# Optimization experiments

Hardware: AMD Instinct MI355X
Metric: run time of the kernel (lower is better)

The kernel has to match this reference:

```python
import jax, jax.numpy as jnp
import numpy as np

EPS = 1e-5

def _bn(x, g, b, m, v):
    # inference batchnorm: (x - mean) * rsqrt(var + eps) * gamma + beta
    return (x - m) * jax.lax.rsqrt(v + EPS) * g + b

def _relu6(x):
    return jnp.clip(x, 0.0, 6.0)

def setup_inputs() -> dict:
    key = jax.random.key(0)
    ks = jax.random.split(key, 20)
    N, Cin, Cout, K = 200000, 32, 32, 9  # K = 3^2 kernel offsets (dimension=2)
    H = int(round(Cin * 6))              # hidden = in_channels * expand_ratio = 192
    inp = {}
    inp["feats"] = jax.random.normal(ks[0], (N, Cin), jnp.float32)
    # rulebook neighbor map: -1 means no active neighbor at that kernel offset
    inp["neighbor_idx"] = jax.random.randint(ks[1], (N, K), -1, N, dtype=jnp.int32)
    # ME convs have bias=False by default
    inp["W1"] = jax.random.normal(ks[2], (Cin, H), jnp.float32) * 0.05
    inp["W2"] = jax.random.normal(ks[3], (K, H), jnp.float32) * 0.05   # channelwise (depthwise) kernel
    inp["W3"] = jax.random.normal(ks[4], (H, Cout), jnp.float32) * 0.05
    for i, (name, c) in enumerate([("1", H), ("2", H), ("3", Cout)]):
        base = 5 + 4 * i
        inp["g" + name] = 1.0 + 0.1 * jax.random.normal(ks[base], (c,), jnp.float32)
        inp["b" + name] = 0.1 * jax.random.normal(ks[base + 1], (c,), jnp.float32)
        inp["m" + name] = 0.1 * jax.random.normal(ks[base + 2], (c,), jnp.float32)
        inp["v" + name] = jax.random.uniform(ks[base + 3], (c,), jnp.float32, 0.5, 1.5)
    return inp

def _depthwise_sparse_conv(x, neighbor_idx, W2):
    # x: [N, H], neighbor_idx: [N, K] (-1 = missing), W2: [K, H]
    K = W2.shape[0]
    acc = jnp.zeros_like(x)
    safe = jnp.maximum(neighbor_idx, 0)
    valid = (neighbor_idx >= 0)
    for k in range(K):  # small fixed kernel loop; each gather streams [N, H]
        g = jnp.where(valid[:, k:k + 1], x[safe[:, k]], 0.0)
        acc = acc + g * W2[k]
    return acc

def reference(feats, neighbor_idx, W1, W2, W3,
              g1, b1, m1, v1, g2, b2, m2, v2, g3, b3, m3, v3):
    identity = feats
    x = _relu6(_bn(feats @ W1, g1, b1, m1, v1))          # 1x1 expand conv
    x = _depthwise_sparse_conv(x, neighbor_idx, W2)       # 3x3 depthwise sparse conv
    x = _relu6(_bn(x, g2, b2, m2, v2))
    x = _bn(x @ W3, g3, b3, m3, v3)                       # 1x1 project conv
    return x + identity                                   # residual (in==out, stride==1)
```

## Files before the change

### kernel.cpp

```cpp
#include <hip/hip_runtime.h>

#define EPS 1e-5f

typedef __bf16 bf16x8 __attribute__((ext_vector_type(8)));
typedef float f32x4 __attribute__((ext_vector_type(4)));

union BF8 { bf16x8 v; unsigned short u[8]; uint4 q; };

__device__ inline unsigned short f32_to_bf16(float f) {
    unsigned u = __builtin_bit_cast(unsigned, f);
    return (unsigned short)((u + 0x7FFFu + ((u >> 16) & 1u)) >> 16);
}
__device__ inline float relu6f(float x) { return fminf(fmaxf(x, 0.f), 6.f); }

__global__ __launch_bounds__(256) void k0_prep(
    const float* __restrict__ W1, const float* __restrict__ W3,
    const float* __restrict__ g1, const float* __restrict__ b1,
    const float* __restrict__ m1, const float* __restrict__ v1,
    const float* __restrict__ g2, const float* __restrict__ b2,
    const float* __restrict__ m2, const float* __restrict__ v2,
    const float* __restrict__ g3, const float* __restrict__ b3,
    const float* __restrict__ m3, const float* __restrict__ v3,
    unsigned short* __restrict__ w1t, unsigned short* __restrict__ w3t,
    float* __restrict__ bnc)
{
    const int gtid = blockIdx.x * 256 + threadIdx.x;
    const int gstr = gridDim.x * 256;
    for (int i = gtid; i < 6144; i += gstr) {
        int n = i >> 5, k = i & 31;
        w1t[i] = f32_to_bf16(W1[k * 192 + n]);
    }
    for (int i = gtid; i < 6144; i += gstr) {
        int n = i / 192, k = i - n * 192;
        w3t[i] = f32_to_bf16(W3[k * 32 + n]);
    }
    if (blockIdx.x == 0) {
        int t = threadIdx.x;
        const float Q = 255.f / 6.f;
        if (t < 192) {
            float s = g1[t] * rsqrtf(v1[t] + EPS);
            bnc[t] = s * Q; bnc[192 + t] = (b1[t] - m1[t] * s) * Q;
            float u = g2[t] * rsqrtf(v2[t] + EPS);
            bnc[384 + t] = u; bnc[576 + t] = b2[t] - m2[t] * u;
            if (t < 32) {
                float w = g3[t] * rsqrtf(v3[t] + EPS);
                bnc[768 + t] = w; bnc[800 + t] = b3[t] - m3[t] * w;
            }
        }
    }
}

__global__ __launch_bounds__(256) void k1_expand(
    const float* __restrict__ feats, const unsigned short* __restrict__ w1t,
    const float* __restrict__ bnc, unsigned char* __restrict__ x1, int N)
{
    __shared__ __align__(16) unsigned outB[128 * 52];
    const int tid = threadIdx.x;
    const int rowbase = blockIdx.x * 128;
    const int lane = tid & 63, wave = tid >> 6;
    const int m = lane & 15, q = lane >> 4;

    bf16x8 bf[12];
#pragma unroll
    for (int t = 0; t < 12; ++t)
        bf[t] = *(const bf16x8*)(w1t + (16 * t + m) * 32 + q * 8);

#pragma unroll
    for (int p = 0; p < 2; ++p) {
        const int tile = wave * 2 + p;
        const int row = rowbase + tile * 16 + m;
        float4 f0 = {0.f,0.f,0.f,0.f}, f1 = {0.f,0.f,0.f,0.f};
        if (row < N) {
            f0 = *(const float4*)(feats + (size_t)row * 32 + q * 8);
            f1 = *(const float4*)(feats + (size_t)row * 32 + q * 8 + 4);
        }
        BF8 af;
        af.u[0] = f32_to_bf16(f0.x); af.u[1] = f32_to_bf16(f0.y);
        af.u[2] = f32_to_bf16(f0.z); af.u[3] = f32_to_bf16(f0.w);
        af.u[4] = f32_to_bf16(f1.x); af.u[5] = f32_to_bf16(f1.y);
        af.u[6] = f32_to_bf16(f1.z); af.u[7] = f32_to_bf16(f1.w);

        f32x4 acc[12];
#pragma unroll
        for (int t = 0; t < 12; ++t) {
            f32x4 z = {0.f, 0.f, 0.f, 0.f};
            acc[t] = __builtin_amdgcn_mfma_f32_16x16x32_bf16(bf[t], af.v, z, 0, 0, 0);
        }

        const int rl = tile * 16 + m;
#pragma unroll
        for (int t = 0; t < 12; ++t) {
            float4 sv = *(const float4*)(bnc + 16 * t + 4 * q);
            float4 bv = *(const float4*)(bnc + 192 + 16 * t + 4 * q);
            float y0 = fminf(fmaxf(fmaf(acc[t][0], sv.x, bv.x), 0.f), 255.f);
            float y1 = fminf(fmaxf(fmaf(acc[t][1], sv.y, bv.y), 0.f), 255.f);
            float y2 = fminf(fmaxf(fmaf(acc[t][2], sv.z, bv.z), 0.f), 255.f);
            float y3 = fminf(fmaxf(fmaf(acc[t][3], sv.w, bv.w), 0.f), 255.f);
            unsigned d = (unsigned)(y0 + 0.5f)
                       | ((unsigned)(y1 + 0.5f) << 8)
                       | ((unsigned)(y2 + 0.5f) << 16)
                       | ((unsigned)(y3 + 0.5f) << 24);
            outB[rl * 52 + 4 * t + q] = d;
        }
    }
    __syncthreads();

#pragma unroll
    for (int j = 0; j < 6; ++j) {
        int i = j * 256 + tid;
        int r = i / 12, c = i % 12;
        int gr = rowbase + r;
        if (gr < N)
            *(uint4*)(x1 + (size_t)gr * 192 + c * 16) = *(const uint4*)(&outB[r * 52 + c * 4]);
    }
}

__global__ __launch_bounds__(192) void k2_fused(
    const unsigned char* __restrict__ x1, const int* __restrict__ nbr,
    const float* __restrict__ W2, const unsigned short* __restrict__ w3t,
    const float* __restrict__ bnc, const float* __restrict__ feats,
    float* __restrict__ out, int N)
{
    __shared__ __align__(16) unsigned short x2L[48 * 200];
    __shared__ __align__(16) int offL[48 * 12];
    const int tid = threadIdx.x;
    const int rowbase = blockIdx.x * 48;

    for (int i = tid; i < 432; i += 192) {
        int r = i / 9, k = i - r * 9;
        int n = rowbase + r;
        int idx = (n < N) ? nbr[(size_t)n * 9 + k] : -1;
        offL[r * 12 + k] = (idx < 0) ? -1 : idx * 192;
    }

    const int cg = tid % 48;
    const int slot = tid / 48;
    const int c0 = cg * 4;
    const char* x1b = (const char*)x1 + c0;

    const float DQ = 6.f / 255.f;
    float w2v[9][4];
#pragma unroll
    for (int k = 0; k < 9; ++k) {
        float4 w = *(const float4*)(W2 + k * 192 + c0);
        w2v[k][0] = w.x * DQ; w2v[k][1] = w.y * DQ; w2v[k][2] = w.z * DQ; w2v[k][3] = w.w * DQ;
    }
    float4 s2 = *(const float4*)(bnc + 384 + c0);
    float4 bb2 = *(const float4*)(bnc + 576 + c0);
    __syncthreads();

#pragma unroll
    for (int it = 0; it < 6; ++it) {
        int r0 = it * 8 + slot, r1 = r0 + 4;
        const int* nA = &offL[r0 * 12];
        const int* nB = &offL[r1 * 12];
        int4 a03 = *(const int4*)nA; int4 a47 = *(const int4*)(nA + 4); int a8 = nA[8];
        int4 b03 = *(const int4*)nB; int4 b47 = *(const int4*)(nB + 4); int b8 = nB[8];
        int offA[9] = {a03.x, a03.y, a03.z, a03.w, a47.x, a47.y, a47.z, a47.w, a8};
        int offB[9] = {b03.x, b03.y, b03.z, b03.w, b47.x, b47.y, b47.z, b47.w, b8};
        unsigned gA[9], gB[9];
#pragma unroll
        for (int k = 0; k < 9; ++k) {
            gA[k] = *(const unsigned*)(x1b + (offA[k] < 0 ? 0 : offA[k]));
            gB[k] = *(const unsigned*)(x1b + (offB[k] < 0 ? 0 : offB[k]));
        }
        float a0 = 0.f, a1 = 0.f, a2 = 0.f, a3 = 0.f;
        float c0f = 0.f, c1 = 0.f, c2 = 0.f, c3 = 0.f;
#pragma unroll
        for (int k = 0; k < 9; ++k) {
            unsigned ga = offA[k] >= 0 ? gA[k] : 0u;
            unsigned gb = offB[k] >= 0 ? gB[k] : 0u;
            a0 = fmaf((float)(ga & 0xFF),         w2v[k][0], a0);
            a1 = fmaf((float)((ga >> 8) & 0xFF),  w2v[k][1], a1);
            a2 = fmaf((float)((ga >> 16) & 0xFF), w2v[k][2], a2);
            a3 = fmaf((float)(ga >> 24),          w2v[k][3], a3);
            c0f = fmaf((float)(gb & 0xFF),         w2v[k][0], c0f);
            c1  = fmaf((float)((gb >> 8) & 0xFF),  w2v[k][1], c1);
            c2  = fmaf((float)((gb >> 16) & 0xFF), w2v[k][2], c2);
            c3  = fmaf((float)(gb >> 24),          w2v[k][3], c3);
        }
        a0 = relu6f(fmaf(a0, s2.x, bb2.x));
        a1 = relu6f(fmaf(a1, s2.y, bb2.y));
        a2 = relu6f(fmaf(a2, s2.z, bb2.z));
        a3 = relu6f(fmaf(a3, s2.w, bb2.w));
        c0f = relu6f(fmaf(c0f, s2.x, bb2.x));
        c1  = relu6f(fmaf(c1,  s2.y, bb2.y));
        c2  = relu6f(fmaf(c2,  s2.z, bb2.z));
        c3  = relu6f(fmaf(c3,  s2.w, bb2.w));
        uint2 pA, pB;
        pA.x = (unsigned)f32_to_bf16(a0) | ((unsigned)f32_to_bf16(a1) << 16);
        pA.y = (unsigned)f32_to_bf16(a2) | ((unsigned)f32_to_bf16(a3) << 16);
        pB.x = (unsigned)f32_to_bf16(c0f) | ((unsigned)f32_to_bf16(c1) << 16);
        pB.y = (unsigned)f32_to_bf16(c2)  | ((unsigned)f32_to_bf16(c3) << 16);
        *(uint2*)(&x2L[r0 * 200 + c0]) = pA;
        *(uint2*)(&x2L[r1 * 200 + c0]) = pB;
    }
    __syncthreads();

    const int lane = tid & 63;
    const int wave = tid >> 6;
    const int m = lane & 15;
    const int q = lane >> 4;

    bf16x8 bfrag[12];
#pragma unroll
    for (int s = 0; s < 6; ++s)
#pragma unroll
        for (int t = 0; t < 2; ++t)
            bfrag[s * 2 + t] = *(const bf16x8*)(w3t + (16 * t + m) * 192 + 32 * s + q * 8);

    f32x4 acc0 = {0.f, 0.f, 0.f, 0.f}, acc1 = {0.f, 0.f, 0.f, 0.f};
    const int rw = wave * 16;
#pragma unroll
    for (int s = 0; s < 6; ++s) {
        bf16x8 a = *reinterpret_cast<const bf16x8*>(&x2L[(rw + m) * 200 + 32 * s + q * 8]);
        acc0 = __builtin_amdgcn_mfma_f32_16x16x32_bf16(a, bfrag[s * 2 + 0], acc0, 0, 0, 0);
        acc1 = __builtin_amdgcn_mfma_f32_16x16x32_bf16(a, bfrag[s * 2 + 1], acc1, 0, 0, 0);
    }

#pragma unroll
    for (int t = 0; t < 2; ++t) {
        f32x4 acc = (t == 0) ? acc0 : acc1;
        int c = 16 * t + m;
        float s3 = bnc[768 + c], bb3 = bnc[800 + c];
#pragma unroll
        for (int i = 0; i < 4; ++i) {
            int r = rowbase + rw + q * 4 + i;
            if (r < N) {
                int o = r * 32 + c;
                out[o] = fmaf(acc[i], s3, bb3) + feats[o];
            }
        }
    }
}

extern "C" void kernel_launch(void* const* d_in, const int* in_sizes, int n_in,
                              void* d_out, int out_size, void* d_ws, size_t ws_size,
                              hipStream_t stream) {
    const float* feats = (const float*)d_in[0];
    const int*   nbr   = (const int*)d_in[1];
    const float* W1    = (const float*)d_in[2];
    const float* W2    = (const float*)d_in[3];
    const float* W3    = (const float*)d_in[4];
    const float* g1 = (const float*)d_in[5];
    const float* b1 = (const float*)d_in[6];
    const float* m1 = (const float*)d_in[7];
    const float* v1 = (const float*)d_in[8];
    const float* g2 = (const float*)d_in[9];
    const float* b2 = (const float*)d_in[10];
    const float* m2 = (const float*)d_in[11];
    const float* v2 = (const float*)d_in[12];
    const float* g3 = (const float*)d_in[13];
    const float* b3 = (const float*)d_in[14];
    const float* m3 = (const float*)d_in[15];
    const float* v3 = (const float*)d_in[16];
    float* out = (float*)d_out;

    const int N = in_sizes[0] / 32;

    char* ws = (char*)d_ws;
    unsigned char*  x1  = (unsigned char*)ws;
    unsigned short* w1t = (unsigned short*)(ws + (size_t)N * 192);
    unsigned short* w3t = w1t + 6144;
    float*          bnc = (float*)(w3t + 6144);

    k0_prep<<<dim3(32), dim3(256), 0, stream>>>(
        W1, W3, g1, b1, m1, v1, g2, b2, m2, v2, g3, b3, m3, v3, w1t, w3t, bnc);
    k1_expand<<<dim3((N + 127) / 128), dim3(256), 0, stream>>>(
        feats, w1t, bnc, x1, N);
    k2_fused<<<dim3((N + 47) / 48), dim3(192), 0, stream>>>(
        x1, nbr, W2, w3t, bnc, feats, out, N);
}
```

Measured before the change: 200.5 us.

## Fuse prep, expand and depthwise/project kernels into one cooperative persistent kernel

Replaces the three kernel launches with a single cooperative persistent kernel. Each block first computes the BN constants and bf16 weight fragments itself, runs a grid-stride expand phase into the uint8 workspace, does a grid-wide sync, then runs the gather, depthwise and project phase grid-stride. The aim is to remove launch gaps and the separate prep kernel. In exchange it adds a grid barrier, tiles phase one at 96 rows with 192 threads, and recomputes the weight conversion in every block.

```diff
diff --git a/kernel.cpp b/kernel.cpp
--- a/kernel.cpp
+++ b/kernel.cpp
@@ -1,4 +1,7 @@
 #include <hip/hip_runtime.h>
+#include <hip/hip_cooperative_groups.h>
+
+namespace coopg = cooperative_groups;
 
 #define EPS 1e-5f
 
@@ -13,129 +16,101 @@
 }
 __device__ inline float relu6f(float x) { return fminf(fmaxf(x, 0.f), 6.f); }
 
-__global__ __launch_bounds__(256) void k0_prep(
-    const float* __restrict__ W1, const float* __restrict__ W3,
+__global__ __launch_bounds__(192) void fused(
+    const float* __restrict__ feats, const int* __restrict__ nbr,
+    const float* __restrict__ W1, const float* __restrict__ W2,
+    const float* __restrict__ W3,
     const float* __restrict__ g1, const float* __restrict__ b1,
     const float* __restrict__ m1, const float* __restrict__ v1,
     const float* __restrict__ g2, const float* __restrict__ b2,
     const float* __restrict__ m2, const float* __restrict__ v2,
     const float* __restrict__ g3, const float* __restrict__ b3,
     const float* __restrict__ m3, const float* __restrict__ v3,
-    unsigned short* __restrict__ w1t, unsigned short* __restrict__ w3t,
-    float* __restrict__ bnc)
+    unsigned char* __restrict__ x1, float* __restrict__ out,
+    int N, int nt1, int nt2)
 {
-    const int gtid = blockIdx.x * 256 + threadIdx.x;
-    const int gstr = gridDim.x * 256;
-    for (int i = gtid; i < 6144; i += gstr) {
-        int n = i >> 5, k = i & 31;
-        w1t[i] = f32_to_bf16(W1[k * 192 + n]);
-    }
-    for (int i = gtid; i < 6144; i += gstr) {
-        int n = i / 192, k = i - n * 192;
-        w3t[i] = f32_to_bf16(W3[k * 32 + n]);
-    }
-    if (blockIdx.x == 0) {
-        int t = threadIdx.x;
-        const float Q = 255.f / 6.f;
-        if (t < 192) {
-            float s = g1[t] * rsqrtf(v1[t] + EPS);
-            bnc[t] = s * Q; bnc[192 + t] = (b1[t] - m1[t] * s) * Q;
-            float u = g2[t] * rsqrtf(v2[t] + EPS);
-            bnc[384 + t] = u; bnc[576 + t] = b2[t] - m2[t] * u;
-            if (t < 32) {
-                float w = g3[t] * rsqrtf(v3[t] + EPS);
-                bnc[768 + t] = w; bnc[800 + t] = b3[t] - m3[t] * w;
-            }
-        }
-    }
-}
-
-__global__ __launch_bounds__(256) void k1_expand(
-    const float* __restrict__ feats, const unsigned short* __restrict__ w1t,
-    const float* __restrict__ bnc, unsigned char* __restrict__ x1, int N)
-{
-    __shared__ __align__(16) unsigned outB[128 * 52];
-    const int tid = threadIdx.x;
-    const int rowbase = blockIdx.x * 128;
+    __shared__ __align__(16) char sh[21504];
+    unsigned*       outB = (unsigned*)sh;
+    float*          bn1  = (float*)(sh + 19968);
+    unsigned short* x2L  = (unsigned short*)sh;
+    int*            offL = (int*)(sh + 19200);
+
+    const int tid  = threadIdx.x;
     const int lane = tid & 63, wave = tid >> 6;
     const int m = lane & 15, q = lane >> 4;
 
-    bf16x8 bf[12];
+    {
+        const float Q = 255.f / 6.f;
+        int c = tid;
+        float s = g1[c] * rsqrtf(v1[c] + EPS);
+        bn1[c]       = s * Q;
+        bn1[192 + c] = (b1[c] - m1[c] * s) * Q;
+    }
+    BF8 bf[12];
 #pragma unroll
     for (int t = 0; t < 12; ++t)
-        bf[t] = *(const bf16x8*)(w1t + (16 * t + m) * 32 + q * 8);
-
-#pragma unroll
-    for (int p = 0; p < 2; ++p) {
-        const int tile = wave * 2 + p;
-        const int row = rowbase + tile * 16 + m;
-        float4 f0 = {0.f,0.f,0.f,0.f}, f1 = {0.f,0.f,0.f,0.f};
-        if (row < N) {
-            f0 = *(const float4*)(feats + (size_t)row * 32 + q * 8);
-            f1 = *(const float4*)(feats + (size_t)row * 32 + q * 8 + 4);
-        }
-        BF8 af;
-        af.u[0] = f32_to_bf16(f0.x); af.u[1] = f32_to_bf16(f0.y);
-        af.u[2] = f32_to_bf16(f0.z); af.u[3] = f32_to_bf16(f0.w);
-        af.u[4] = f32_to_bf16(f1.x); af.u[5] = f32_to_bf16(f1.y);
-        af.u[6] = f32_to_bf16(f1.z); af.u[7] = f32_to_bf16(f1.w);
-
-        f32x4 acc[12];
-#pragma unroll
-        for (int t = 0; t < 12; ++t) {
-            f32x4 z = {0.f, 0.f, 0.f, 0.f};
-            acc[t] = __builtin_amdgcn_mfma_f32_16x16x32_bf16(bf[t], af.v, z, 0, 0, 0);
-        }
-
-        const int rl = tile * 16 + m;
-#pragma unroll
-        for (int t = 0; t < 12; ++t) {
-            float4 sv = *(const float4*)(bnc + 16 * t + 4 * q);
-            float4 bv = *(const float4*)(bnc + 192 + 16 * t + 4 * q);
-            float y0 = fminf(fmaxf(fmaf(acc[t][0], sv.x, bv.x), 0.f), 255.f);
-            float y1 = fminf(fmaxf(fmaf(acc[t][1], sv.y, bv.y), 0.f), 255.f);
-            float y2 = fminf(fmaxf(fmaf(acc[t][2], sv.z, bv.z), 0.f), 255.f);
-            float y3 = fminf(fmaxf(fmaf(acc[t][3], sv.w, bv.w), 0.f), 255.f);
-            unsigned d = (unsigned)(y0 + 0.5f)
-                       | ((unsigned)(y1 + 0.5f) << 8)
-                       | ((unsigned)(y2 + 0.5f) << 16)
-                       | ((unsigned)(y3 + 0.5f) << 24);
-            outB[rl * 52 + 4 * t + q] = d;
-        }
-    }
+#pragma unroll
+        for (int j = 0; j < 8; ++j)
+            bf[t].u[j] = f32_to_bf16(W1[(q * 8 + j) * 192 + 16 * t + m]);
     __syncthreads();
 
-#pragma unroll
-    for (int j = 0; j < 6; ++j) {
-        int i = j * 256 + tid;
-        int r = i / 12, c = i % 12;
-        int gr = rowbase + r;
-        if (gr < N)
-            *(uint4*)(x1 + (size_t)gr * 192 + c * 16) = *(const uint4*)(&outB[r * 52 + c * 4]);
-    }
-}
-
-__global__ __launch_bounds__(192) void k2_fused(
-    const unsigned char* __restrict__ x1, const int* __restrict__ nbr,
-    const float* __restrict__ W2, const unsigned short* __restrict__ w3t,
-    const float* __restrict__ bnc, const float* __restrict__ feats,
-    float* __restrict__ out, int N)
-{
-    __shared__ __align__(16) unsigned short x2L[48 * 200];
-    __shared__ __align__(16) int offL[48 * 12];
-    const int tid = threadIdx.x;
-    const int rowbase = blockIdx.x * 48;
-
-    for (int i = tid; i < 432; i += 192) {
-        int r = i / 9, k = i - r * 9;
-        int n = rowbase + r;
-        int idx = (n < N) ? nbr[(size_t)n * 9 + k] : -1;
-        offL[r * 12 + k] = (idx < 0) ? -1 : idx * 192;
-    }
-
-    const int cg = tid % 48;
+    for (int tb = blockIdx.x; tb < nt1; tb += gridDim.x) {
+        const int rowbase = tb * 96;
+#pragma unroll
+        for (int p = 0; p < 2; ++p) {
+            const int tile = wave * 2 + p;
+            const int row = rowbase + tile * 16 + m;
+            float4 f0 = {0.f,0.f,0.f,0.f}, f1 = {0.f,0.f,0.f,0.f};
+            if (row < N) {
+                f0 = *(const float4*)(feats + (size_t)row * 32 + q * 8);
+                f1 = *(const float4*)(feats + (size_t)row * 32 + q * 8 + 4);
+            }
+            BF8 af;
+            af.u[0] = f32_to_bf16(f0.x); af.u[1] = f32_to_bf16(f0.y);
+            af.u[2] = f32_to_bf16(f0.z); af.u[3] = f32_to_bf16(f0.w);
+            af.u[4] = f32_to_bf16(f1.x); af.u[5] = f32_to_bf16(f1.y);
+            af.u[6] = f32_to_bf16(f1.z); af.u[7] = f32_to_bf16(f1.w);
+
+            f32x4 acc[12];
+#pragma unroll
+            for (int t = 0; t < 12; ++t) {
+                f32x4 z = {0.f, 0.f, 0.f, 0.f};
+                acc[t] = __builtin_amdgcn_mfma_f32_16x16x32_bf16(bf[t].v, af.v, z, 0, 0, 0);
+            }
+
+            const int rl = tile * 16 + m;
+#pragma unroll
+            for (int t = 0; t < 12; ++t) {
+                float4 sv = *(const float4*)(bn1 + 16 * t + 4 * q);
+                float4 bv = *(const float4*)(bn1 + 192 + 16 * t + 4 * q);
+                float y0 = fminf(fmaxf(fmaf(acc[t][0], sv.x, bv.x), 0.f), 255.f);
+                float y1 = fminf(fmaxf(fmaf(acc[t][1], sv.y, bv.y), 0.f), 255.f);
+                float y2 = fminf(fmaxf(fmaf(acc[t][2], sv.z, bv.z), 0.f), 255.f);
+                float y3 = fminf(fmaxf(fmaf(acc[t][3], sv.w, bv.w), 0.f), 255.f);
+                unsigned d = (unsigned)(y0 + 0.5f)
+                           | ((unsigned)(y1 + 0.5f) << 8)
+                           | ((unsigned)(y2 + 0.5f) << 16)
+                           | ((unsigned)(y3 + 0.5f) << 24);
+                outB[rl * 52 + 4 * t + q] = d;
+            }
+        }
+        __syncthreads();
+#pragma unroll
+        for (int j = 0; j < 6; ++j) {
+            int i = j * 192 + tid;
+            int r = i / 12, c = i % 12;
+            int gr = rowbase + r;
+            if (gr < N)
+                *(uint4*)(x1 + (size_t)gr * 192 + c * 16) = *(const uint4*)(&outB[r * 52 + c * 4]);
+        }
+        __syncthreads();
+    }
+
+    coopg::this_grid().sync();
+
+    const int cg48 = tid % 48;
     const int slot = tid / 48;
-    const int c0 = cg * 4;
+    const int c0 = cg48 * 4;
     const char* x1b = (const char*)x1 + c0;
 
     const float DQ = 6.f / 255.f;
@@ -145,90 +120,109 @@
         float4 w = *(const float4*)(W2 + k * 192 + c0);
         w2v[k][0] = w.x * DQ; w2v[k][1] = w.y * DQ; w2v[k][2] = w.z * DQ; w2v[k][3] = w.w * DQ;
     }
-    float4 s2 = *(const float4*)(bnc + 384 + c0);
-    float4 bb2 = *(const float4*)(bnc + 576 + c0);
-    __syncthreads();
-
-#pragma unroll
-    for (int it = 0; it < 6; ++it) {
-        int r0 = it * 8 + slot, r1 = r0 + 4;
-        const int* nA = &offL[r0 * 12];
-        const int* nB = &offL[r1 * 12];
-        int4 a03 = *(const int4*)nA; int4 a47 = *(const int4*)(nA + 4); int a8 = nA[8];
-        int4 b03 = *(const int4*)nB; int4 b47 = *(const int4*)(nB + 4); int b8 = nB[8];
-        int offA[9] = {a03.x, a03.y, a03.z, a03.w, a47.x, a47.y, a47.z, a47.w, a8};
-        int offB[9] = {b03.x, b03.y, b03.z, b03.w, b47.x, b47.y, b47.z, b47.w, b8};
-        unsigned gA[9], gB[9];
-#pragma unroll
-        for (int k = 0; k < 9; ++k) {
-            gA[k] = *(const unsigned*)(x1b + (offA[k] < 0 ? 0 : offA[k]));
-            gB[k] = *(const unsigned*)(x1b + (offB[k] < 0 ? 0 : offB[k]));
-        }
-        float a0 = 0.f, a1 = 0.f, a2 = 0.f, a3 = 0.f;
-        float c0f = 0.f, c1 = 0.f, c2 = 0.f, c3 = 0.f;
-#pragma unroll
-        for (int k = 0; k < 9; ++k) {
-            unsigned ga = offA[k] >= 0 ? gA[k] : 0u;
-            unsigned gb = offB[k] >= 0 ? gB[k] : 0u;
-            a0 = fmaf((float)(ga & 0xFF),         w2v[k][0], a0);
-            a1 = fmaf((float)((ga >> 8) & 0xFF),  w2v[k][1], a1);
-            a2 = fmaf((float)((ga >> 16) & 0xFF), w2v[k][2], a2);
-            a3 = fmaf((float)(ga >> 24),          w2v[k][3], a3);
-            c0f = fmaf((float)(gb & 0xFF),         w2v[k][0], c0f);
-            c1  = fmaf((float)((gb >> 8) & 0xFF),  w2v[k][1], c1);
-            c2  = fmaf((float)((gb >> 16) & 0xFF), w2v[k][2], c2);
-            c3  = fmaf((float)(gb >> 24),          w2v[k][3], c3);
-        }
-        a0 = relu6f(fmaf(a0, s2.x, bb2.x));
-        a1 = relu6f(fmaf(a1, s2.y, bb2.y));
-        a2 = relu6f(fmaf(a2, s2.z, bb2.z));
-        a3 = relu6f(fmaf(a3, s2.w, bb2.w));
-        c0f = relu6f(fmaf(c0f, s2.x, bb2.x));
-        c1  = relu6f(fmaf(c1,  s2.y, bb2.y));
-        c2  = relu6f(fmaf(c2,  s2.z, bb2.z));
-        c3  = relu6f(fmaf(c3,  s2.w, bb2.w));
-        uint2 pA, pB;
-        pA.x = (unsigned)f32_to_bf16(a0) | ((unsigned)f32_to_bf16(a1) << 16);
-        pA.y = (unsigned)f32_to_bf16(a2) | ((unsigned)f32_to_bf16(a3) << 16);
-        pB.x = (unsigned)f32_to_bf16(c0f) | ((unsigned)f32_to_bf16(c1) << 16);
-        pB.y = (unsigned)f32_to_bf16(c2)  | ((unsigned)f32_to_bf16(c3) << 16);
-        *(uint2*)(&x2L[r0 * 200 + c0]) = pA;
-        *(uint2*)(&x2L[r1 * 200 + c0]) = pB;
-    }
-    __syncthreads();
-
-    const int lane = tid & 63;
-    const int wave = tid >> 6;
-    const int m = lane & 15;
-    const int q = lane >> 4;
-
-    bf16x8 bfrag[12];
+    float4 s2, bb2;
+    {
+        float4 gv = *(const float4*)(g2 + c0), bv = *(const float4*)(b2 + c0);
+        float4 mv = *(const float4*)(m2 + c0), vv = *(const float4*)(v2 + c0);
+        s2.x = gv.x * rsqrtf(vv.x + EPS); bb2.x = bv.x - mv.x * s2.x;
+        s2.y = gv.y * rsqrtf(vv.y + EPS); bb2.y = bv.y - mv.y * s2.y;
+        s2.z = gv.z * rsqrtf(vv.z + EPS); bb2.z = bv.z - mv.z * s2.z;
+        s2.w = gv.w * rsqrtf(vv.w + EPS); bb2.w = bv.w - mv.w * s2.w;
+    }
+    BF8 bfrag[12];
 #pragma unroll
     for (int s = 0; s < 6; ++s)
 #pragma unroll
         for (int t = 0; t < 2; ++t)
-            bfrag[s * 2 + t] = *(const bf16x8*)(w3t + (16 * t + m) * 192 + 32 * s + q * 8);
-
-    f32x4 acc0 = {0.f, 0.f, 0.f, 0.f}, acc1 = {0.f, 0.f, 0.f, 0.f};
-    const int rw = wave * 16;
-#pragma unroll
-    for (int s = 0; s < 6; ++s) {
-        bf16x8 a = *reinterpret_cast<const bf16x8*>(&x2L[(rw + m) * 200 + 32 * s + q * 8]);
-        acc0 = __builtin_amdgcn_mfma_f32_16x16x32_bf16(a, bfrag[s * 2 + 0], acc0, 0, 0, 0);
-        acc1 = __builtin_amdgcn_mfma_f32_16x16x32_bf16(a, bfrag[s * 2 + 1], acc1, 0, 0, 0);
-    }
-
+#pragma unroll
+            for (int j = 0; j < 8; ++j)
+                bfrag[s * 2 + t].u[j] = f32_to_bf16(W3[(32 * s + q * 8 + j) * 32 + 16 * t + m]);
+    float s3v[2], bb3v[2];
 #pragma unroll
     for (int t = 0; t < 2; ++t) {
-        f32x4 acc = (t == 0) ? acc0 : acc1;
         int c = 16 * t + m;
-        float s3 = bnc[768 + c], bb3 = bnc[800 + c];
-#pragma unroll
-        for (int i = 0; i < 4; ++i) {
-            int r = rowbase + rw + q * 4 + i;
-            if (r < N) {
-                int o = r * 32 + c;
-                out[o] = fmaf(acc[i], s3, bb3) + feats[o];
+        float w = g3[c] * rsqrtf(v3[c] + EPS);
+        s3v[t] = w; bb3v[t] = b3[c] - m3[c] * w;
+    }
+
+    for (int tb = blockIdx.x; tb < nt2; tb += gridDim.x) {
+        const int rowbase = tb * 48;
+        for (int i = tid; i < 432; i += 192) {
+            int r = i / 9, k = i - r * 9;
+            int n = rowbase + r;
+            int idx = (n < N) ? nbr[(size_t)n * 9 + k] : -1;
+            offL[r * 12 + k] = (idx < 0) ? -1 : idx * 192;
+        }
+        __syncthreads();
+
+#pragma unroll
+        for (int it = 0; it < 6; ++it) {
+            int r0 = it * 8 + slot, r1 = r0 + 4;
+            const int* nA = &offL[r0 * 12];
+            const int* nB = &offL[r1 * 12];
+            int4 a03 = *(const int4*)nA; int4 a47 = *(const int4*)(nA + 4); int a8 = nA[8];
+            int4 b03 = *(const int4*)nB; int4 b47 = *(const int4*)(nB + 4); int b8 = nB[8];
+            int offA[9] = {a03.x, a03.y, a03.z, a03.w, a47.x, a47.y, a47.z, a47.w, a8};
+            int offB[9] = {b03.x, b03.y, b03.z, b03.w, b47.x, b47.y, b47.z, b47.w, b8};
+            unsigned gA[9], gB[9];
+#pragma unroll
+            for (int k = 0; k < 9; ++k) {
+                gA[k] = *(const unsigned*)(x1b + (offA[k] < 0 ? 0 : offA[k]));
+                gB[k] = *(const unsigned*)(x1b + (offB[k] < 0 ? 0 : offB[k]));
+            }
+            float a0 = 0.f, a1 = 0.f, a2 = 0.f, a3 = 0.f;
+            float c0f = 0.f, c1 = 0.f, c2 = 0.f, c3 = 0.f;
+#pragma unroll
+            for (int k = 0; k < 9; ++k) {
+                unsigned ga = offA[k] >= 0 ? gA[k] : 0u;
+                unsigned gb = offB[k] >= 0 ? gB[k] : 0u;
+                a0 = fmaf((float)(ga & 0xFF),         w2v[k][0], a0);
+                a1 = fmaf((float)((ga >> 8) & 0xFF),  w2v[k][1], a1);
+                a2 = fmaf((float)((ga >> 16) & 0xFF), w2v[k][2], a2);
+                a3 = fmaf((float)(ga >> 24),          w2v[k][3], a3);
+                c0f = fmaf((float)(gb & 0xFF),         w2v[k][0], c0f);
+                c1  = fmaf((float)((gb >> 8) & 0xFF),  w2v[k][1], c1);
+                c2  = fmaf((float)((gb >> 16) & 0xFF), w2v[k][2], c2);
+                c3  = fmaf((float)(gb >> 24),          w2v[k][3], c3);
+            }
+            a0 = relu6f(fmaf(a0, s2.x, bb2.x));
+            a1 = relu6f(fmaf(a1, s2.y, bb2.y));
+            a2 = relu6f(fmaf(a2, s2.z, bb2.z));
+            a3 = relu6f(fmaf(a3, s2.w, bb2.w));
+            c0f = relu6f(fmaf(c0f, s2.x, bb2.x));
+            c1  = relu6f(fmaf(c1,  s2.y, bb2.y));
+            c2  = relu6f(fmaf(c2,  s2.z, bb2.z));
+            c3  = relu6f(fmaf(c3,  s2.w, bb2.w));
+            uint2 pA, pB;
+            pA.x = (unsigned)f32_to_bf16(a0) | ((unsigned)f32_to_bf16(a1) << 16);
+            pA.y = (unsigned)f32_to_bf16(a2) | ((unsigned)f32_to_bf16(a3) << 16);
+            pB.x = (unsigned)f32_to_bf16(c0f) | ((unsigned)f32_to_bf16(c1) << 16);
+            pB.y = (unsigned)f32_to_bf16(c2)  | ((unsigned)f32_to_bf16(c3) << 16);
+            *(uint2*)(&x2L[r0 * 200 + c0]) = pA;
+            *(uint2*)(&x2L[r1 * 200 + c0]) = pB;
+        }
+        __syncthreads();
+
+        f32x4 acc0 = {0.f, 0.f, 0.f, 0.f}, acc1 = {0.f, 0.f, 0.f, 0.f};
+        const int rw = wave * 16;
+#pragma unroll
+        for (int s = 0; s < 6; ++s) {
+            bf16x8 a = *reinterpret_cast<const bf16x8*>(&x2L[(rw + m) * 200 + 32 * s + q * 8]);
+            acc0 = __builtin_amdgcn_mfma_f32_16x16x32_bf16(a, bfrag[s * 2 + 0].v, acc0, 0, 0, 0);
+            acc1 = __builtin_amdgcn_mfma_f32_16x16x32_bf16(a, bfrag[s * 2 + 1].v, acc1, 0, 0, 0);
+        }
+
+#pragma unroll
+        for (int t = 0; t < 2; ++t) {
+            f32x4 acc = (t == 0) ? acc0 : acc1;
+            int c = 16 * t + m;
+#pragma unroll
+            for (int i = 0; i < 4; ++i) {
+                int r = rowbase + rw + q * 4 + i;
+                if (r < N) {
+                    int o = r * 32 + c;
+                    out[o] = fmaf(acc[i], s3v[t], bb3v[t]) + feats[o];
+                }
             }
         }
     }
@@ -257,17 +251,30 @@
     float* out = (float*)d_out;
 
     const int N = in_sizes[0] / 32;
-
-    char* ws = (char*)d_ws;
-    unsigned char*  x1  = (unsigned char*)ws;
-    unsigned short* w1t = (unsigned short*)(ws + (size_t)N * 192);
-    unsigned short* w3t = w1t + 6144;
-    float*          bnc = (float*)(w3t + 6144);
-
-    k0_prep<<<dim3(32), dim3(256), 0, stream>>>(
-        W1, W3, g1, b1, m1, v1, g2, b2, m2, v2, g3, b3, m3, v3, w1t, w3t, bnc);
-    k1_expand<<<dim3((N + 127) / 128), dim3(256), 0, stream>>>(
-        feats, w1t, bnc, x1, N);
-    k2_fused<<<dim3((N + 47) / 48), dim3(192), 0, stream>>>(
-        x1, nbr, W2, w3t, bnc, feats, out, N);
+    int nt1 = (N + 95) / 96;
+    int nt2 = (N + 47) / 48;
+
+    unsigned char* x1 = (unsigned char*)d_ws;
+
+    static int s_grid = -1;
+    if (s_grid < 0) {
+        int dev = 0; hipGetDevice(&dev);
+        int cus = 256;
+        hipDeviceGetAttribute(&cus, hipDeviceAttributeMultiprocessorCount, dev);
+        int occ = 0;
+        hipOccupancyMaxActiveBlocksPerMultiprocessor(&occ, fused, 192, 0);
+        if (occ < 1) occ = 1;
+        s_grid = occ * cus;
+    }
+    int maxt = (nt1 > nt2) ? nt1 : nt2;
+    int grid = (s_grid < maxt) ? s_grid : maxt;
+
+    void* args[] = {
+        (void*)&feats, (void*)&nbr, (void*)&W1, (void*)&W2, (void*)&W3,
+        (void*)&g1, (void*)&b1, (void*)&m1, (void*)&v1,
+        (void*)&g2, (void*)&b2, (void*)&m2, (void*)&v2,
+        (void*)&g3, (void*)&b3, (void*)&m3, (void*)&v3,
+        (void*)&x1, (void*)&out, (void*)&N, (void*)&nt1, (void*)&nt2
+    };
+    hipLaunchCooperativeKernel(fused, dim3(grid), dim3(192), args, 0u, stream);
 }
```

After: 327.1 us. 63.2% more time.

## Drop prep kernel and compute weight conversion and BN constants in consumer kernels

Applied to the files above, without the earlier changes.

Removes the separate k0_prep launch and instead converts W1/W3 to bf16 and folds the batchnorm constants inside each block of the expand and fused kernels. The expand kernel also drops its LDS staging buffer and writes packed uint8 activations straight to global memory with 4-byte stores. This saves one kernel launch and its serialization, but adds redundant strided weight loads and conversions in every block and replaces coalesced 16-byte stores with narrower scattered ones.

```diff
diff --git a/kernel.cpp b/kernel.cpp
--- a/kernel.cpp
+++ b/kernel.cpp
@@ -13,57 +13,32 @@
 }
 __device__ inline float relu6f(float x) { return fminf(fmaxf(x, 0.f), 6.f); }
 
-__global__ __launch_bounds__(256) void k0_prep(
-    const float* __restrict__ W1, const float* __restrict__ W3,
+__global__ __launch_bounds__(256) void k1_expand(
+    const float* __restrict__ feats, const float* __restrict__ W1,
     const float* __restrict__ g1, const float* __restrict__ b1,
     const float* __restrict__ m1, const float* __restrict__ v1,
-    const float* __restrict__ g2, const float* __restrict__ b2,
-    const float* __restrict__ m2, const float* __restrict__ v2,
-    const float* __restrict__ g3, const float* __restrict__ b3,
-    const float* __restrict__ m3, const float* __restrict__ v3,
-    unsigned short* __restrict__ w1t, unsigned short* __restrict__ w3t,
-    float* __restrict__ bnc)
+    unsigned char* __restrict__ x1, int N)
 {
-    const int gtid = blockIdx.x * 256 + threadIdx.x;
-    const int gstr = gridDim.x * 256;
-    for (int i = gtid; i < 6144; i += gstr) {
-        int n = i >> 5, k = i & 31;
-        w1t[i] = f32_to_bf16(W1[k * 192 + n]);
-    }
-    for (int i = gtid; i < 6144; i += gstr) {
-        int n = i / 192, k = i - n * 192;
-        w3t[i] = f32_to_bf16(W3[k * 32 + n]);
-    }
-    if (blockIdx.x == 0) {
-        int t = threadIdx.x;
-        const float Q = 255.f / 6.f;
-        if (t < 192) {
-            float s = g1[t] * rsqrtf(v1[t] + EPS);
-            bnc[t] = s * Q; bnc[192 + t] = (b1[t] - m1[t] * s) * Q;
-            float u = g2[t] * rsqrtf(v2[t] + EPS);
-            bnc[384 + t] = u; bnc[576 + t] = b2[t] - m2[t] * u;
-            if (t < 32) {
-                float w = g3[t] * rsqrtf(v3[t] + EPS);
-                bnc[768 + t] = w; bnc[800 + t] = b3[t] - m3[t] * w;
-            }
-        }
-    }
-}
-
-__global__ __launch_bounds__(256) void k1_expand(
-    const float* __restrict__ feats, const unsigned short* __restrict__ w1t,
-    const float* __restrict__ bnc, unsigned char* __restrict__ x1, int N)
-{
-    __shared__ __align__(16) unsigned outB[128 * 52];
+    __shared__ __align__(16) float bn1[384];
     const int tid = threadIdx.x;
     const int rowbase = blockIdx.x * 128;
     const int lane = tid & 63, wave = tid >> 6;
     const int m = lane & 15, q = lane >> 4;
 
-    bf16x8 bf[12];
+    if (tid < 192) {
+        const float Q = 255.f / 6.f;
+        float s = g1[tid] * rsqrtf(v1[tid] + EPS);
+        bn1[tid]       = s * Q;
+        bn1[192 + tid] = (b1[tid] - m1[tid] * s) * Q;
+    }
+
+    BF8 bf[12];
 #pragma unroll
     for (int t = 0; t < 12; ++t)
-        bf[t] = *(const bf16x8*)(w1t + (16 * t + m) * 32 + q * 8);
+#pragma unroll
+        for (int j = 0; j < 8; ++j)
+            bf[t].u[j] = f32_to_bf16(W1[(q * 8 + j) * 192 + 16 * t + m]);
+    __syncthreads();
 
 #pragma unroll
     for (int p = 0; p < 2; ++p) {
@@ -84,42 +59,37 @@
 #pragma unroll
         for (int t = 0; t < 12; ++t) {
             f32x4 z = {0.f, 0.f, 0.f, 0.f};
-            acc[t] = __builtin_amdgcn_mfma_f32_16x16x32_bf16(bf[t], af.v, z, 0, 0, 0);
-        }
-
-        const int rl = tile * 16 + m;
-#pragma unroll
-        for (int t = 0; t < 12; ++t) {
-            float4 sv = *(const float4*)(bnc + 16 * t + 4 * q);
-            float4 bv = *(const float4*)(bnc + 192 + 16 * t + 4 * q);
-            float y0 = fminf(fmaxf(fmaf(acc[t][0], sv.x, bv.x), 0.f), 255.f);
-            float y1 = fminf(fmaxf(fmaf(acc[t][1], sv.y, bv.y), 0.f), 255.f);
-            float y2 = fminf(fmaxf(fmaf(acc[t][2], sv.z, bv.z), 0.f), 255.f);
-            float y3 = fminf(fmaxf(fmaf(acc[t][3], sv.w, bv.w), 0.f), 255.f);
-            unsigned d = (unsigned)(y0 + 0.5f)
-                       | ((unsigned)(y1 + 0.5f) << 8)
-                       | ((unsigned)(y2 + 0.5f) << 16)
-                       | ((unsigned)(y3 + 0.5f) << 24);
-            outB[rl * 52 + 4 * t + q] = d;
-        }
-    }
-    __syncthreads();
-
-#pragma unroll
-    for (int j = 0; j < 6; ++j) {
-        int i = j * 256 + tid;
-        int r = i / 12, c = i % 12;
-        int gr = rowbase + r;
-        if (gr < N)
-            *(uint4*)(x1 + (size_t)gr * 192 + c * 16) = *(const uint4*)(&outB[r * 52 + c * 4]);
+            acc[t] = __builtin_amdgcn_mfma_f32_16x16x32_bf16(bf[t].v, af.v, z, 0, 0, 0);
+        }
+
+        if (row < N) {
+            unsigned char* xr = x1 + (size_t)row * 192 + 4 * q;
+#pragma unroll
+            for (int t = 0; t < 12; ++t) {
+                float4 sv = *(const float4*)(bn1 + 16 * t + 4 * q);
+                float4 bv = *(const float4*)(bn1 + 192 + 16 * t + 4 * q);
+                float y0 = fminf(fmaxf(fmaf(acc[t][0], sv.x, bv.x), 0.f), 255.f);
+                float y1 = fminf(fmaxf(fmaf(acc[t][1], sv.y, bv.y), 0.f), 255.f);
+                float y2 = fminf(fmaxf(fmaf(acc[t][2], sv.z, bv.z), 0.f), 255.f);
+                float y3 = fminf(fmaxf(fmaf(acc[t][3], sv.w, bv.w), 0.f), 255.f);
+                unsigned d = (unsigned)(y0 + 0.5f)
+                           | ((unsigned)(y1 + 0.5f) << 8)
+                           | ((unsigned)(y2 + 0.5f) << 16)
+                           | ((unsigned)(y3 + 0.5f) << 24);
+                *(unsigned*)(xr + 16 * t) = d;
+            }
+        }
     }
 }
 
 __global__ __launch_bounds__(192) void k2_fused(
     const unsigned char* __restrict__ x1, const int* __restrict__ nbr,
-    const float* __restrict__ W2, const unsigned short* __restrict__ w3t,
-    const float* __restrict__ bnc, const float* __restrict__ feats,
-    float* __restrict__ out, int N)
+    const float* __restrict__ W2, const float* __restrict__ W3,
+    const float* __restrict__ g2, const float* __restrict__ b2,
+    const float* __restrict__ m2, const float* __restrict__ v2,
+    const float* __restrict__ g3, const float* __restrict__ b3,
+    const float* __restrict__ m3, const float* __restrict__ v3,
+    const float* __restrict__ feats, float* __restrict__ out, int N)
 {
     __shared__ __align__(16) unsigned short x2L[48 * 200];
     __shared__ __align__(16) int offL[48 * 12];
@@ -145,8 +115,15 @@
         float4 w = *(const float4*)(W2 + k * 192 + c0);
         w2v[k][0] = w.x * DQ; w2v[k][1] = w.y * DQ; w2v[k][2] = w.z * DQ; w2v[k][3] = w.w * DQ;
     }
-    float4 s2 = *(const float4*)(bnc + 384 + c0);
-    float4 bb2 = *(const float4*)(bnc + 576 + c0);
+    float4 s2, bb2;
+    {
+        float4 gv = *(const float4*)(g2 + c0), bv = *(const float4*)(b2 + c0);
+        float4 mv = *(const float4*)(m2 + c0), vv = *(const float4*)(v2 + c0);
+        s2.x = gv.x * rsqrtf(vv.x + EPS); bb2.x = bv.x - mv.x * s2.x;
+        s2.y = gv.y * rsqrtf(vv.y + EPS); bb2.y = bv.y - mv.y * s2.y;
+        s2.z = gv.z * rsqrtf(vv.z + EPS); bb2.z = bv.z - mv.z * s2.z;
+        s2.w = gv.w * rsqrtf(vv.w + EPS); bb2.w = bv.w - mv.w * s2.w;
+    }
     __syncthreads();
 
 #pragma unroll
@@ -202,27 +179,30 @@
     const int m = lane & 15;
     const int q = lane >> 4;
 
-    bf16x8 bfrag[12];
+    BF8 bfrag[12];
 #pragma unroll
     for (int s = 0; s < 6; ++s)
 #pragma unroll
         for (int t = 0; t < 2; ++t)
-            bfrag[s * 2 + t] = *(const bf16x8*)(w3t + (16 * t + m) * 192 + 32 * s + q * 8);
+#pragma unroll
+            for (int j = 0; j < 8; ++j)
+                bfrag[s * 2 + t].u[j] = f32_to_bf16(W3[(32 * s + q * 8 + j) * 32 + 16 * t + m]);
 
     f32x4 acc0 = {0.f, 0.f, 0.f, 0.f}, acc1 = {0.f, 0.f, 0.f, 0.f};
     const int rw = wave * 16;
 #pragma unroll
     for (int s = 0; s < 6; ++s) {
         bf16x8 a = *reinterpret_cast<const bf16x8*>(&x2L[(rw + m) * 200 + 32 * s + q * 8]);
-        acc0 = __builtin_amdgcn_mfma_f32_16x16x32_bf16(a, bfrag[s * 2 + 0], acc0, 0, 0, 0);
-        acc1 = __builtin_amdgcn_mfma_f32_16x16x32_bf16(a, bfrag[s * 2 + 1], acc1, 0, 0, 0);
+        acc0 = __builtin_amdgcn_mfma_f32_16x16x32_bf16(a, bfrag[s * 2 + 0].v, acc0, 0, 0, 0);
+        acc1 = __builtin_amdgcn_mfma_f32_16x16x32_bf16(a, bfrag[s * 2 + 1].v, acc1, 0, 0, 0);
     }
 
 #pragma unroll
     for (int t = 0; t < 2; ++t) {
         f32x4 acc = (t == 0) ? acc0 : acc1;
         int c = 16 * t + m;
-        float s3 = bnc[768 + c], bb3 = bnc[800 + c];
+        float w = g3[c] * rsqrtf(v3[c] + EPS);
+        float s3 = w, bb3 = b3[c] - m3[c] * w;
 #pragma unroll
         for (int i = 0; i < 4; ++i) {
             int r = rowbase + rw + q * 4 + i;
@@ -258,16 +238,10 @@
 
     const int N = in_sizes[0] / 32;
 
-    char* ws = (char*)d_ws;
-    unsigned char*  x1  = (unsigned char*)ws;
-    unsigned short* w1t = (unsigned short*)(ws + (size_t)N * 192);
-    unsigned short* w3t = w1t + 6144;
-    float*          bnc = (float*)(w3t + 6144);
-
-    k0_prep<<<dim3(32), dim3(256), 0, stream>>>(
-        W1, W3, g1, b1, m1, v1, g2, b2, m2, v2, g3, b3, m3, v3, w1t, w3t, bnc);
+    unsigned char* x1 = (unsigned char*)d_ws;
+
     k1_expand<<<dim3((N + 127) / 128), dim3(256), 0, stream>>>(
-        feats, w1t, bnc, x1, N);
+        feats, W1, g1, b1, m1, v1, x1, N);
     k2_fused<<<dim3((N + 47) / 48), dim3(192), 0, stream>>>(
-        x1, nbr, W2, w3t, bnc, feats, out, N);
-}
+        x1, nbr, W2, W3, g2, b2, m2, v2, g3, b3, m3, v3, feats, out, N);
+}
```

New measurement: 204.7 us. 1.02x slower.
